# Optimization experiments

Hardware: AMD Instinct MI355X
Metric: run time of the kernel (lower is better)

The kernel has to match this reference:

```python
import jax, jax.numpy as jnp
import numpy as np

B, S, D, H = 2, 2048, 1024, 16
DK = D // H
NEG = -1e9


def setup_inputs() -> dict:
    key = jax.random.key(0)
    ks = jax.random.split(key, 12)
    inp = {
        "query": jax.random.normal(ks[0], (B, S, D), jnp.float32),
        "key": jax.random.normal(ks[1], (B, S, D), jnp.float32),
        "value": jax.random.normal(ks[2], (B, S, D), jnp.float32),
        "mask": jax.random.randint(ks[3], (B, S), 0, 2, jnp.int32),
    }
    # 4 linears (q, k, v, out), each d_model x d_model with bias.
    scale = 1.0 / np.sqrt(D)
    for i, name in enumerate(["wq", "wk", "wv", "wo"]):
        inp[name] = jax.random.uniform(ks[4 + i], (D, D), jnp.float32, -scale, scale)
        inp["b" + name[1]] = jax.random.uniform(ks[8 + i], (D,), jnp.float32, -scale, scale)
    return inp


def _split_heads(x):  # [B,S,D] -> [B,H,S,DK]
    return x.reshape(B, S, H, DK).transpose(0, 2, 1, 3)


def reference(query, key, value, mask, wq, bq, wk, bk, wv, bv, wo, bo):
    q = _split_heads(query @ wq.T + bq)
    k = _split_heads(key @ wk.T + bk)
    v = _split_heads(value @ wv.T + bv)
    scores = jnp.einsum("bhqd,bhkd->bhqk", q, k) / jnp.sqrt(jnp.float32(DK))
    # mask: [B,S] -> [B,1,1,S]; masked_fill where mask == 0
    m = mask[:, None, None, :]
    scores = jnp.where(m == 0, NEG, scores)
    attn = jax.nn.softmax(scores, axis=-1)  # dropout p=0 (eval) -> identity
    x = jnp.einsum("bhqk,bhkd->bhqd", attn, v)
    x = x.transpose(0, 2, 1, 3).reshape(B, S, D)
    return x @ wo.T + bo
```

## Files before the change

kernel.cpp:

```cpp
#include <hip/hip_runtime.h>


typedef _Float16 f16;
typedef _Float16 f16x8 __attribute__((ext_vector_type(8)));
typedef _Float16 f16x4 __attribute__((ext_vector_type(4)));
typedef __fp16 fp16x2r __attribute__((ext_vector_type(2)));
typedef float f32x4 __attribute__((ext_vector_type(4)));

union F16x4u { f16x4 v; fp16x2r h[2]; };

#define MFMA_F16(a, b, c) __builtin_amdgcn_mfma_f32_16x16x32_f16((a), (b), (c), 0, 0, 0)
#define MFMA16(a, b, c) __builtin_amdgcn_mfma_f32_16x16x16f16((a), (b), (c), 0, 0, 0)
#define L2E 1.44269504088896340736f

__device__ __forceinline__ void gld16(const void* g, void* l) {
    __builtin_amdgcn_global_load_lds(
        (__attribute__((address_space(1))) void*)(g),
        (__attribute__((address_space(3))) void*)(l), 16, 0, 0);
}

__global__ __launch_bounds__(256) void cvt_kernel(
    const float* __restrict__ q, const float* __restrict__ k,
    const float* __restrict__ v,
    const float* __restrict__ wq, const float* __restrict__ wk,
    const float* __restrict__ wv, const float* __restrict__ wo,
    f16* __restrict__ oq, f16* __restrict__ ok, f16* __restrict__ ov,
    f16* __restrict__ owq, f16* __restrict__ owk, f16* __restrict__ owv,
    f16* __restrict__ owo)
{
    const int z = blockIdx.y;
    const float* src;
    f16* dst;
    int n;
    switch (z) {
        case 0: src = q;  dst = oq;  n = 4194304; break;
        case 1: src = k;  dst = ok;  n = 4194304; break;
        case 2: src = v;  dst = ov;  n = 4194304; break;
        case 3: src = wq; dst = owq; n = 1048576; break;
        case 4: src = wk; dst = owk; n = 1048576; break;
        case 5: src = wv; dst = owv; n = 1048576; break;
        default: src = wo; dst = owo; n = 1048576; break;
    }
    int idx = (blockIdx.x * 256 + threadIdx.x) * 8;
    if (idx >= n) return;
    float4 a = *(const float4*)(src + idx);
    float4 b = *(const float4*)(src + idx + 4);
    f16x8 h = { (f16)a.x, (f16)a.y, (f16)a.z, (f16)a.w,
                (f16)b.x, (f16)b.y, (f16)b.z, (f16)b.w };
    *(f16x8*)(dst + idx) = h;
}

__global__ __launch_bounds__(256) void proj_qkv_kernel(
    const f16* __restrict__ xq, const f16* __restrict__ xk,
    const f16* __restrict__ xv,
    const f16* __restrict__ wqh, const f16* __restrict__ wkh,
    const f16* __restrict__ wvh,
    const float* __restrict__ bq, const float* __restrict__ bk,
    const float* __restrict__ bv,
    f16* __restrict__ qh, f16* __restrict__ kh, f16* __restrict__ vt)
{
    const int z = blockIdx.z;
    const f16* X = (z == 0) ? xq : (z == 1) ? xk : xv;
    const f16* W = (z == 0) ? wqh : (z == 1) ? wkh : wvh;
    const float* bias = (z == 0) ? bq : (z == 1) ? bk : bv;
    const f16* P0 = (z < 2) ? W : X;
    const f16* P1 = (z < 2) ? X : W;

    __shared__ __align__(16) f16 smem[16384];
    f16* As = smem;
    f16* Bs = smem + 8192;
    f16* L  = smem;

    const int t = threadIdx.x;
    const int wave = t >> 6, lane = t & 63, quad = lane >> 4, l15 = lane & 15;
    const int m_base = (wave >> 1) * 64, n_base = (wave & 1) * 64;
    const int blockM = (z < 2) ? blockIdx.y * 128 : blockIdx.x * 128;
    const int blockN = (z < 2) ? blockIdx.x * 128 : blockIdx.y * 128;

    const int srow = lane >> 3;
    const int sblk = (lane & 7) ^ srow;

    f32x4 acc[4][4];
#pragma unroll
    for (int mt = 0; mt < 4; mt++)
#pragma unroll
        for (int nt = 0; nt < 4; nt++)
            acc[mt][nt] = (f32x4){0.f, 0.f, 0.f, 0.f};

    for (int k0 = 0; k0 < 1024; k0 += 64) {
        __syncthreads();
#pragma unroll
        for (int j = 0; j < 4; j++) {
            int r0 = wave * 32 + j * 8;
            gld16(&P0[(size_t)(blockM + r0 + srow) * 1024 + k0 + sblk * 8],
                  &As[r0 * 64]);
            gld16(&P1[(size_t)(blockN + r0 + srow) * 1024 + k0 + sblk * 8],
                  &Bs[r0 * 64]);
        }
        __syncthreads();

#pragma unroll
        for (int c = 0; c < 2; c++) {
            f16x8 af[4], bf[4];
#pragma unroll
            for (int mt = 0; mt < 4; mt++)
                af[mt] = *(const f16x8*)(&As[(m_base + mt * 16 + l15) * 64 +
                                             (((c * 4 + quad) ^ (l15 & 7)) << 3)]);
#pragma unroll
            for (int nt = 0; nt < 4; nt++)
                bf[nt] = *(const f16x8*)(&Bs[(n_base + nt * 16 + l15) * 64 +
                                             (((c * 4 + quad) ^ (l15 & 7)) << 3)]);
#pragma unroll
            for (int mt = 0; mt < 4; mt++)
#pragma unroll
                for (int nt = 0; nt < 4; nt++)
                    acc[mt][nt] = MFMA_F16(af[mt], bf[nt], acc[mt][nt]);
        }
    }

    if (z < 2) {
        f16* o = (z == 0) ? qh : kh;
        const float scale = (z == 0) ? 0.125f * L2E : 1.0f;
        float4 b4[4];
#pragma unroll
        for (int mt = 0; mt < 4; mt++)
            b4[mt] = *(const float4*)(&bias[blockM + m_base + mt * 16 + quad * 4]);

#pragma unroll
        for (int half = 0; half < 2; half++) {
            __syncthreads();
            if ((wave & 1) == half) {
#pragma unroll
                for (int mt = 0; mt < 4; mt++)
#pragma unroll
                    for (int nt = 0; nt < 4; nt++) {
                        f16x4 pk = {
                            (f16)((acc[mt][nt][0] + b4[mt].x) * scale),
                            (f16)((acc[mt][nt][1] + b4[mt].y) * scale),
                            (f16)((acc[mt][nt][2] + b4[mt].z) * scale),
                            (f16)((acc[mt][nt][3] + b4[mt].w) * scale) };
                        *(f16x4*)(&L[(nt * 16 + l15) * 136 +
                                     m_base + mt * 16 + quad * 4]) = pk;
                    }
            }
            __syncthreads();
#pragma unroll
            for (int pass = 0; pass < 4; pass++) {
                int unit = pass * 32 + (t >> 3);
                int hh = unit >> 6, s_loc = unit & 63;
                f16x8 vv = *(const f16x8*)(&L[s_loc * 136 + hh * 64 + (t & 7) * 8]);
                int s_glob = blockN + half * 64 + s_loc;
                int b = s_glob >> 11, s = s_glob & 2047;
                int h_glob = (blockM >> 6) + hh;
                *(f16x8*)(&o[(((size_t)(b * 16 + h_glob) * 2048 + s) << 6) +
                             (t & 7) * 8]) = vv;
            }
        }
    } else {
        float bv_[4];
#pragma unroll
        for (int nt = 0; nt < 4; nt++)
            bv_[nt] = bias[blockN + n_base + nt * 16 + l15];

#pragma unroll
        for (int half = 0; half < 2; half++) {
            __syncthreads();
            if ((wave & 1) == half) {
#pragma unroll
                for (int mt = 0; mt < 4; mt++)
#pragma unroll
                    for (int nt = 0; nt < 4; nt++) {
                        f16x4 pk = { (f16)(acc[mt][nt][0] + bv_[nt]),
                                     (f16)(acc[mt][nt][1] + bv_[nt]),
                                     (f16)(acc[mt][nt][2] + bv_[nt]),
                                     (f16)(acc[mt][nt][3] + bv_[nt]) };
                        *(f16x4*)(&L[(nt * 16 + l15) * 136 +
                                     m_base + mt * 16 + quad * 4]) = pk;
                    }
            }
            __syncthreads();
#pragma unroll
            for (int pass = 0; pass < 4; pass++) {
                int f_loc = pass * 16 + (t >> 4);
                f16x8 vv = *(const f16x8*)(&L[f_loc * 136 + (t & 15) * 8]);
                int feat = blockN + half * 64 + f_loc;
                int hh = feat >> 6, dk = feat & 63;
                int b = blockM >> 11;
                int s0 = (blockM & 2047) + (t & 15) * 8;
                *(f16x8*)(&vt[((size_t)((b * 16 + hh) * 64 + dk) << 11) + s0]) = vv;
            }
        }
    }
}

__device__ __forceinline__ void flash_stage(
    const f16* kbase, const f16* vbase, int key0,
    f16* Kb, f16* Vb, int wave, int srow8, int sblk)
{
#pragma unroll
    for (int p = 0; p < 2; p++) {
        int r0 = p * 32 + wave * 8;
        int row = r0 + srow8;
        gld16(&kbase[(size_t)(key0 + row) * 64 + sblk * 8], &Kb[r0 * 64]);
        gld16(&vbase[(size_t)row * 2048 + key0 + sblk * 8], &Vb[r0 * 64]);
    }
}

__device__ __forceinline__ void flash_phase(
    const f16* Kbuf, const f16* Vbuf, const float* bias_all, int key0,
    const f16x8 (&qf)[2][2], int quad, int l15,
    f32x4 (&O)[2][4], f32x4 (&lacc)[2])
{
    f32x4 sc[2][4];
#pragma unroll
    for (int nt = 0; nt < 4; nt++) {
        const f16* krow = &Kbuf[(nt * 16 + l15) * 64];
        f16x8 kf0 = *(const f16x8*)(&krow[(quad ^ (l15 & 7)) << 3]);
        f16x8 kf1 = *(const f16x8*)(&krow[((quad + 4) ^ (l15 & 7)) << 3]);
        float4 b4 = *(const float4*)(&bias_all[key0 + nt * 16 + quad * 4]);
#pragma unroll
        for (int cb = 0; cb < 2; cb++) {
            f32x4 z4 = (f32x4){b4.x, b4.y, b4.z, b4.w};
            z4 = MFMA_F16(kf0, qf[cb][0], z4);
            sc[cb][nt] = MFMA_F16(kf1, qf[cb][1], z4);
        }
    }
    const f16x4 ones = {(f16)1.f, (f16)1.f, (f16)1.f, (f16)1.f};
    f16x4 pf[2][4];
#pragma unroll
    for (int cb = 0; cb < 2; cb++)
#pragma unroll
        for (int nt = 0; nt < 4; nt++) {
            float p0 = exp2f(sc[cb][nt][0]);
            float p1 = exp2f(sc[cb][nt][1]);
            float p2 = exp2f(sc[cb][nt][2]);
            float p3 = exp2f(sc[cb][nt][3]);
            F16x4u u;
            u.h[0] = __builtin_amdgcn_cvt_pkrtz(p0, p1);
            u.h[1] = __builtin_amdgcn_cvt_pkrtz(p2, p3);
            pf[cb][nt] = u.v;
            lacc[cb] = MFMA16(ones, pf[cb][nt], lacc[cb]);
        }
#pragma unroll
    for (int nto = 0; nto < 4; nto++) {
        const f16* vrow = &Vbuf[(nto * 16 + l15) * 64];
#pragma unroll
        for (int nt = 0; nt < 4; nt++) {
            f16x4 vf = *(const f16x4*)(&vrow[
                (((nt * 2 + (quad >> 1)) ^ (l15 & 7)) << 3) + (quad & 1) * 4]);
            O[0][nto] = MFMA16(vf, pf[0][nt], O[0][nto]);
            O[1][nto] = MFMA16(vf, pf[1][nt], O[1][nto]);
        }
    }
}

__global__ __launch_bounds__(256) void flash_kernel(
    const f16* __restrict__ qh, const f16* __restrict__ kh,
    const f16* __restrict__ vt, const int* __restrict__ mask,
    f16* __restrict__ ctx)
{
    __shared__ __align__(16) f16 Ks0[64 * 64];
    __shared__ __align__(16) f16 Ks1[64 * 64];
    __shared__ __align__(16) f16 Vts0[64 * 64];
    __shared__ __align__(16) f16 Vts1[64 * 64];
    __shared__ float bias_all[2048];

    const int t = threadIdx.x;
    const int wave = t >> 6, lane = t & 63, quad = lane >> 4, l15 = lane & 15;
    const int bh = blockIdx.x;
    const int b = bh >> 4, h = bh & 15;
    const int q0 = blockIdx.y * 128;

    const f16* qbase = qh + (size_t)bh * (2048 * 64);
    const f16* kbase = kh + (size_t)bh * (2048 * 64);
    const f16* vbase = vt + (size_t)bh * (64 * 2048);

#pragma unroll
    for (int j = 0; j < 8; j++) {
        int i = j * 256 + t;
        bias_all[i] = (mask[b * 2048 + i] == 0) ? -1.0e9f : 0.0f;
    }

    f16x8 qf[2][2];
#pragma unroll
    for (int cb = 0; cb < 2; cb++) {
        int qrow = q0 + wave * 32 + cb * 16 + l15;
        qf[cb][0] = *(const f16x8*)(&qbase[qrow * 64 + quad * 8]);
        qf[cb][1] = *(const f16x8*)(&qbase[qrow * 64 + 32 + quad * 8]);
    }

    f32x4 O[2][4];
#pragma unroll
    for (int cb = 0; cb < 2; cb++)
#pragma unroll
        for (int n = 0; n < 4; n++) O[cb][n] = (f32x4){0.f, 0.f, 0.f, 0.f};
    f32x4 lacc[2] = {(f32x4){0.f, 0.f, 0.f, 0.f}, (f32x4){0.f, 0.f, 0.f, 0.f}};

    const int srow8 = lane >> 3;
    const int sblk = (lane & 7) ^ srow8;

    flash_stage(kbase, vbase, 0, Ks0, Vts0, wave, srow8, sblk);

    for (int k2 = 0; k2 < 16; k2++) {
        const int key0 = k2 * 128;
        __syncthreads();
        flash_stage(kbase, vbase, key0 + 64, Ks1, Vts1, wave, srow8, sblk);
        flash_phase(Ks0, Vts0, bias_all, key0, qf, quad, l15, O, lacc);
        __syncthreads();
        if (k2 < 15)
            flash_stage(kbase, vbase, key0 + 128, Ks0, Vts0, wave, srow8, sblk);
        flash_phase(Ks1, Vts1, bias_all, key0 + 64, qf, quad, l15, O, lacc);
    }

#pragma unroll
    for (int cb = 0; cb < 2; cb++) {
        const float inv_l = 1.0f / lacc[cb][0];
        int qrow = q0 + wave * 32 + cb * 16 + l15;
#pragma unroll
        for (int nto = 0; nto < 4; nto++) {
            f16x4 pk = { (f16)(O[cb][nto][0] * inv_l),
                         (f16)(O[cb][nto][1] * inv_l),
                         (f16)(O[cb][nto][2] * inv_l),
                         (f16)(O[cb][nto][3] * inv_l) };
            *(f16x4*)(&ctx[(size_t)(b * 2048 + qrow) * 1024 + h * 64 +
                           nto * 16 + quad * 4]) = pk;
        }
    }
}

__global__ __launch_bounds__(256) void proj_out_kernel(
    const f16* __restrict__ ctx, const f16* __restrict__ woh,
    const float* __restrict__ bo, float* __restrict__ out)
{
    __shared__ __align__(16) f16 As[2][128 * 64];
    __shared__ __align__(16) f16 Bs[2][64 * 64];

    const int t = threadIdx.x;
    const int wave = t >> 6, lane = t & 63, quad = lane >> 4, l15 = lane & 15;
    const int m_base = (wave >> 1) * 64, n_base = (wave & 1) * 32;
    const int blockM = blockIdx.x * 128;
    const int blockN = blockIdx.y * 64;

    const int srow = lane >> 3;
    const int sblk = (lane & 7) ^ srow;

    f32x4 acc[4][2];
#pragma unroll
    for (int mt = 0; mt < 4; mt++)
#pragma unroll
        for (int nt = 0; nt < 2; nt++)
            acc[mt][nt] = (f32x4){0.f, 0.f, 0.f, 0.f};

#pragma unroll
    for (int j = 0; j < 4; j++) {
        int r0 = wave * 32 + j * 8;
        gld16(&ctx[(size_t)(blockM + r0 + srow) * 1024 + sblk * 8],
              &As[0][r0 * 64]);
    }
#pragma unroll
    for (int j = 0; j < 2; j++) {
        int r0 = wave * 16 + j * 8;
        gld16(&woh[(size_t)(blockN + r0 + srow) * 1024 + sblk * 8],
              &Bs[0][r0 * 64]);
    }

    for (int ki = 0; ki < 16; ki++) {
        const int cur = ki & 1;
        __syncthreads();

        if (ki < 15) {
            const int k0n = (ki + 1) * 64;
#pragma unroll
            for (int j = 0; j < 4; j++) {
                int r0 = wave * 32 + j * 8;
                gld16(&ctx[(size_t)(blockM + r0 + srow) * 1024 + k0n + sblk * 8],
                      &As[cur ^ 1][r0 * 64]);
            }
#pragma unroll
            for (int j = 0; j < 2; j++) {
                int r0 = wave * 16 + j * 8;
                gld16(&woh[(size_t)(blockN + r0 + srow) * 1024 + k0n + sblk * 8],
                      &Bs[cur ^ 1][r0 * 64]);
            }
        }

#pragma unroll
        for (int c = 0; c < 2; c++) {
            f16x8 af[4], bf[2];
#pragma unroll
            for (int mt = 0; mt < 4; mt++)
                af[mt] = *(const f16x8*)(&As[cur][(m_base + mt * 16 + l15) * 64 +
                                              (((c * 4 + quad) ^ (l15 & 7)) << 3)]);
#pragma unroll
            for (int nt = 0; nt < 2; nt++)
                bf[nt] = *(const f16x8*)(&Bs[cur][(n_base + nt * 16 + l15) * 64 +
                                              (((c * 4 + quad) ^ (l15 & 7)) << 3)]);
#pragma unroll
            for (int mt = 0; mt < 4; mt++)
#pragma unroll
                for (int nt = 0; nt < 2; nt++)
                    acc[mt][nt] = MFMA_F16(af[mt], bf[nt], acc[mt][nt]);
        }
    }

    float bo_[2];
#pragma unroll
    for (int nt = 0; nt < 2; nt++)
        bo_[nt] = bo[blockN + n_base + nt * 16 + l15];

#pragma unroll
    for (int mt = 0; mt < 4; mt++) {
        int row0 = blockM + m_base + mt * 16 + quad * 4;
#pragma unroll
        for (int nt = 0; nt < 2; nt++) {
            int col_g = blockN + n_base + nt * 16 + l15;
#pragma unroll
            for (int i = 0; i < 4; i++)
                out[(size_t)(row0 + i) * 1024 + col_g] = acc[mt][nt][i] + bo_[nt];
        }
    }
}

extern "C" void kernel_launch(void* const* d_in, const int* in_sizes, int n_in,
                              void* d_out, int out_size, void* d_ws, size_t ws_size,
                              hipStream_t stream) {
    const float* query = (const float*)d_in[0];
    const float* key_  = (const float*)d_in[1];
    const float* value = (const float*)d_in[2];
    const int*   mask  = (const int*)d_in[3];
    const float* wq = (const float*)d_in[4];
    const float* bq = (const float*)d_in[5];
    const float* wk = (const float*)d_in[6];
    const float* bk = (const float*)d_in[7];
    const float* wv = (const float*)d_in[8];
    const float* bv = (const float*)d_in[9];
    const float* wo = (const float*)d_in[10];
    const float* bo = (const float*)d_in[11];
    float* out = (float*)d_out;

    f16* xq  = (f16*)d_ws;
    f16* xk  = xq  + 4194304;
    f16* xv  = xk  + 4194304;
    f16* wqh = xv  + 4194304;
    f16* wkh = wqh + 1048576;
    f16* wvh = wkh + 1048576;
    f16* woh = wvh + 1048576;
    f16* qh  = woh + 1048576;
    f16* kh  = qh  + 4194304;
    f16* vt  = kh  + 4194304;
    f16* ctx = xq;

    cvt_kernel<<<dim3(2048, 7), 256, 0, stream>>>(
        query, key_, value, wq, wk, wv, wo, xq, xk, xv, wqh, wkh, wvh, woh);
    proj_qkv_kernel<<<dim3(32, 8, 3), 256, 0, stream>>>(
        xq, xk, xv, wqh, wkh, wvh, bq, bk, bv, qh, kh, vt);
    flash_kernel<<<dim3(32, 16), 256, 0, stream>>>(qh, kh, vt, mask, ctx);
    proj_out_kernel<<<dim3(32, 16), 256, 0, stream>>>(ctx, woh, bo, out);
}
```

Baseline: 237.2 us.

## Split flash attention keys across two wave groups and merge partial sums

The flash kernel now runs 512 threads, with two groups of four waves each taking alternating 64-key halves of every 128-key step. Each group keeps its own double-buffered K/V tiles, and group 1 passes its partial O and row sums to group 0 through LDS for a final merge. The P·V and row-sum MFMAs switch from 16x16x16 to the 16x16x32 f16 instruction by packing two key tiles per operand. This raises waves per block and halves the serial key loop per wave, at the cost of more LDS, an extra reduction pass and more register pressure under launch_bounds(512,4).

```diff
diff --git a/kernel.cpp b/kernel.cpp
--- a/kernel.cpp
+++ b/kernel.cpp
@@ -10,7 +10,6 @@
 union F16x4u { f16x4 v; fp16x2r h[2]; };
 
 #define MFMA_F16(a, b, c) __builtin_amdgcn_mfma_f32_16x16x32_f16((a), (b), (c), 0, 0, 0)
-#define MFMA16(a, b, c) __builtin_amdgcn_mfma_f32_16x16x16f16((a), (b), (c), 0, 0, 0)
 #define L2E 1.44269504088896340736f
 
 __device__ __forceinline__ void gld16(const void* g, void* l) {
@@ -193,20 +192,20 @@
     }
 }
 
-__device__ __forceinline__ void flash_stage(
+__device__ __forceinline__ void flash_stage2(
     const f16* kbase, const f16* vbase, int key0,
-    f16* Kb, f16* Vb, int wave, int srow8, int sblk)
+    f16* Kb, f16* Vb, int wg, int srow8, int sblk)
 {
 #pragma unroll
     for (int p = 0; p < 2; p++) {
-        int r0 = p * 32 + wave * 8;
+        int r0 = wg * 16 + p * 8;
         int row = r0 + srow8;
         gld16(&kbase[(size_t)(key0 + row) * 64 + sblk * 8], &Kb[r0 * 64]);
         gld16(&vbase[(size_t)row * 2048 + key0 + sblk * 8], &Vb[r0 * 64]);
     }
 }
 
-__device__ __forceinline__ void flash_phase(
+__device__ __forceinline__ void flash_phase2(
     const f16* Kbuf, const f16* Vbuf, const float* bias_all, int key0,
     const f16x8 (&qf)[2][2], int quad, int l15,
     f32x4 (&O)[2][4], f32x4 (&lacc)[2])
@@ -225,10 +224,12 @@
             sc[cb][nt] = MFMA_F16(kf1, qf[cb][1], z4);
         }
     }
-    const f16x4 ones = {(f16)1.f, (f16)1.f, (f16)1.f, (f16)1.f};
-    f16x4 pf[2][4];
-#pragma unroll
-    for (int cb = 0; cb < 2; cb++)
+    const f16x8 ones8 = {(f16)1.f, (f16)1.f, (f16)1.f, (f16)1.f,
+                         (f16)1.f, (f16)1.f, (f16)1.f, (f16)1.f};
+    union P8 { f16x8 v8; f16x4 v4[2]; };
+    P8 pp[2][2];
+#pragma unroll
+    for (int cb = 0; cb < 2; cb++) {
 #pragma unroll
         for (int nt = 0; nt < 4; nt++) {
             float p0 = exp2f(sc[cb][nt][0]);
@@ -238,35 +239,38 @@
             F16x4u u;
             u.h[0] = __builtin_amdgcn_cvt_pkrtz(p0, p1);
             u.h[1] = __builtin_amdgcn_cvt_pkrtz(p2, p3);
-            pf[cb][nt] = u.v;
-            lacc[cb] = MFMA16(ones, pf[cb][nt], lacc[cb]);
-        }
+            pp[cb][nt >> 1].v4[nt & 1] = u.v;
+        }
+        lacc[cb] = MFMA_F16(ones8, pp[cb][0].v8, lacc[cb]);
+        lacc[cb] = MFMA_F16(ones8, pp[cb][1].v8, lacc[cb]);
+    }
 #pragma unroll
     for (int nto = 0; nto < 4; nto++) {
         const f16* vrow = &Vbuf[(nto * 16 + l15) * 64];
-#pragma unroll
-        for (int nt = 0; nt < 4; nt++) {
-            f16x4 vf = *(const f16x4*)(&vrow[
-                (((nt * 2 + (quad >> 1)) ^ (l15 & 7)) << 3) + (quad & 1) * 4]);
-            O[0][nto] = MFMA16(vf, pf[0][nt], O[0][nto]);
-            O[1][nto] = MFMA16(vf, pf[1][nt], O[1][nto]);
-        }
-    }
-}
-
-__global__ __launch_bounds__(256) void flash_kernel(
+        P8 va, vb;
+        va.v4[0] = *(const f16x4*)(&vrow[(((quad >> 1) ^ (l15 & 7)) << 3) + (quad & 1) * 4]);
+        va.v4[1] = *(const f16x4*)(&vrow[(((2 + (quad >> 1)) ^ (l15 & 7)) << 3) + (quad & 1) * 4]);
+        vb.v4[0] = *(const f16x4*)(&vrow[(((4 + (quad >> 1)) ^ (l15 & 7)) << 3) + (quad & 1) * 4]);
+        vb.v4[1] = *(const f16x4*)(&vrow[(((6 + (quad >> 1)) ^ (l15 & 7)) << 3) + (quad & 1) * 4]);
+#pragma unroll
+        for (int cb = 0; cb < 2; cb++) {
+            O[cb][nto] = MFMA_F16(va.v8, pp[cb][0].v8, O[cb][nto]);
+            O[cb][nto] = MFMA_F16(vb.v8, pp[cb][1].v8, O[cb][nto]);
+        }
+    }
+}
+
+__global__ __launch_bounds__(512, 4) void flash_kernel(
     const f16* __restrict__ qh, const f16* __restrict__ kh,
     const f16* __restrict__ vt, const int* __restrict__ mask,
     f16* __restrict__ ctx)
 {
-    __shared__ __align__(16) f16 Ks0[64 * 64];
-    __shared__ __align__(16) f16 Ks1[64 * 64];
-    __shared__ __align__(16) f16 Vts0[64 * 64];
-    __shared__ __align__(16) f16 Vts1[64 * 64];
+    __shared__ __align__(16) f16 KV[8 * 4096];
     __shared__ float bias_all[2048];
 
     const int t = threadIdx.x;
     const int wave = t >> 6, lane = t & 63, quad = lane >> 4, l15 = lane & 15;
+    const int group = wave >> 2, wg = wave & 3;
     const int bh = blockIdx.x;
     const int b = bh >> 4, h = bh & 15;
     const int q0 = blockIdx.y * 128;
@@ -275,16 +279,21 @@
     const f16* kbase = kh + (size_t)bh * (2048 * 64);
     const f16* vbase = vt + (size_t)bh * (64 * 2048);
 
-#pragma unroll
-    for (int j = 0; j < 8; j++) {
-        int i = j * 256 + t;
+    f16* K0 = &KV[((0 * 2 + group) * 2 + 0) * 4096];
+    f16* V0 = &KV[((0 * 2 + group) * 2 + 1) * 4096];
+    f16* K1 = &KV[((1 * 2 + group) * 2 + 0) * 4096];
+    f16* V1 = &KV[((1 * 2 + group) * 2 + 1) * 4096];
+
+#pragma unroll
+    for (int j = 0; j < 4; j++) {
+        int i = j * 512 + t;
         bias_all[i] = (mask[b * 2048 + i] == 0) ? -1.0e9f : 0.0f;
     }
 
     f16x8 qf[2][2];
 #pragma unroll
     for (int cb = 0; cb < 2; cb++) {
-        int qrow = q0 + wave * 32 + cb * 16 + l15;
+        int qrow = q0 + wg * 32 + cb * 16 + l15;
         qf[cb][0] = *(const f16x8*)(&qbase[qrow * 64 + quad * 8]);
         qf[cb][1] = *(const f16x8*)(&qbase[qrow * 64 + 32 + quad * 8]);
     }
@@ -299,31 +308,51 @@
     const int srow8 = lane >> 3;
     const int sblk = (lane & 7) ^ srow8;
 
-    flash_stage(kbase, vbase, 0, Ks0, Vts0, wave, srow8, sblk);
-
-    for (int k2 = 0; k2 < 16; k2++) {
-        const int key0 = k2 * 128;
+    flash_stage2(kbase, vbase, group * 64, K0, V0, wg, srow8, sblk);
+
+    for (int k2 = 0; k2 < 16; k2 += 2) {
         __syncthreads();
-        flash_stage(kbase, vbase, key0 + 64, Ks1, Vts1, wave, srow8, sblk);
-        flash_phase(Ks0, Vts0, bias_all, key0, qf, quad, l15, O, lacc);
+        flash_stage2(kbase, vbase, (k2 + 1) * 128 + group * 64, K1, V1,
+                     wg, srow8, sblk);
+        flash_phase2(K0, V0, bias_all, k2 * 128 + group * 64,
+                     qf, quad, l15, O, lacc);
         __syncthreads();
-        if (k2 < 15)
-            flash_stage(kbase, vbase, key0 + 128, Ks0, Vts0, wave, srow8, sblk);
-        flash_phase(Ks1, Vts1, bias_all, key0 + 64, qf, quad, l15, O, lacc);
-    }
-
-#pragma unroll
-    for (int cb = 0; cb < 2; cb++) {
-        const float inv_l = 1.0f / lacc[cb][0];
-        int qrow = q0 + wave * 32 + cb * 16 + l15;
-#pragma unroll
-        for (int nto = 0; nto < 4; nto++) {
-            f16x4 pk = { (f16)(O[cb][nto][0] * inv_l),
-                         (f16)(O[cb][nto][1] * inv_l),
-                         (f16)(O[cb][nto][2] * inv_l),
-                         (f16)(O[cb][nto][3] * inv_l) };
-            *(f16x4*)(&ctx[(size_t)(b * 2048 + qrow) * 1024 + h * 64 +
-                           nto * 16 + quad * 4]) = pk;
+        if (k2 < 14)
+            flash_stage2(kbase, vbase, (k2 + 2) * 128 + group * 64, K0, V0,
+                         wg, srow8, sblk);
+        flash_phase2(K1, V1, bias_all, (k2 + 1) * 128 + group * 64,
+                     qf, quad, l15, O, lacc);
+    }
+
+    __syncthreads();
+    float* Red = (float*)KV;
+    const int t4 = wg * 64 + lane;
+    if (group == 1) {
+#pragma unroll
+        for (int cb = 0; cb < 2; cb++) {
+#pragma unroll
+            for (int nto = 0; nto < 4; nto++)
+                *(f32x4*)(&Red[(cb * 4 + nto) * 1024 + t4 * 4]) = O[cb][nto];
+            Red[8 * 1024 + cb * 256 + t4] = lacc[cb][0];
+        }
+    }
+    __syncthreads();
+    if (group == 0) {
+#pragma unroll
+        for (int cb = 0; cb < 2; cb++) {
+            const float l2 = Red[8 * 1024 + cb * 256 + t4];
+            const float inv_l = 1.0f / (lacc[cb][0] + l2);
+            int qrow = q0 + wg * 32 + cb * 16 + l15;
+#pragma unroll
+            for (int nto = 0; nto < 4; nto++) {
+                f32x4 o2 = *(const f32x4*)(&Red[(cb * 4 + nto) * 1024 + t4 * 4]);
+                f16x4 pk = { (f16)((O[cb][nto][0] + o2[0]) * inv_l),
+                             (f16)((O[cb][nto][1] + o2[1]) * inv_l),
+                             (f16)((O[cb][nto][2] + o2[2]) * inv_l),
+                             (f16)((O[cb][nto][3] + o2[3]) * inv_l) };
+                *(f16x4*)(&ctx[(size_t)(b * 2048 + qrow) * 1024 + h * 64 +
+                               nto * 16 + quad * 4]) = pk;
+            }
         }
     }
 }
@@ -454,6 +483,6 @@
         query, key_, value, wq, wk, wv, wo, xq, xk, xv, wqh, wkh, wvh, woh);
     proj_qkv_kernel<<<dim3(32, 8, 3), 256, 0, stream>>>(
         xq, xk, xv, wqh, wkh, wvh, bq, bk, bv, qh, kh, vt);
-    flash_kernel<<<dim3(32, 16), 256, 0, stream>>>(qh, kh, vt, mask, ctx);
+    flash_kernel<<<dim3(32, 16), 512, 0, stream>>>(qh, kh, vt, mask, ctx);
     proj_out_kernel<<<dim3(32, 16), 256, 0, stream>>>(ctx, woh, bo, out);
 }
```

After: 230.4 us. 1.03x faster.
